# Kernel optimization log

Hardware: AMD Instinct MI355X
Metric: run time of the kernel (lower is better)

## Reference

```python
import jax, jax.numpy as jnp
import numpy as np

B, DEPTH, H, I = 8, 12, 512, 512
N = 2**DEPTH - 1  # 4095 nodes, complete binary tree (heap indexed)


def setup_inputs() -> dict:
    key = jax.random.key(0)
    ks = jax.random.split(key, 9)
    s_i = 1.0 / np.sqrt(I)
    s_h = 1.0 / np.sqrt(H)
    u = lambda k, shape, s: jax.random.uniform(k, shape, jnp.float32, -s, s)
    return {
        "inputs": jax.random.normal(ks[0], (B, N, I), jnp.float32),
        "depth": DEPTH,
        # torch Linear weights stored as [in, out] (already transposed)
        "W_gih": u(ks[1], (I, 3 * H), s_i),
        "b_gih": u(ks[2], (3 * H,), s_i),
        "W_glhh": u(ks[3], (H, 3 * H), s_h),
        "W_grhh": u(ks[4], (H, 3 * H), s_h),
        "W_cih": u(ks[5], (I, H), s_i),
        "b_cih": u(ks[6], (H,), s_i),
        "W_clhh": u(ks[7], (H, H), s_h),
        "W_crhh": u(ks[8], (H, H), s_h),
    }


def reference(inputs, depth, W_gih, b_gih, W_glhh, W_grhh, W_cih, b_cih, W_clhh, W_crhh):
    b, n, _ = inputs.shape
    h_dim = W_clhh.shape[0]
    # Input-dependent affines for every node, computed once (big GEMMs up front).
    gx = inputs @ W_gih + b_gih            # [B, N, 3H]
    cx = inputs @ W_cih + b_cih            # [B, N, H]

    def node_forward(gx_n, cx_n, lh, rh):
        # gates = sigmoid(gate_ih(x) + gate_lhh(lh) + gate_rhh(rh))
        gates = jax.nn.sigmoid(gx_n + lh @ W_glhh + rh @ W_grhh)
        rp, zp, z = jnp.split(gates, 3, axis=-1)
        cell = jnp.tanh(cx_n + (rp * lh) @ W_clhh + (rp * rh) @ W_crhh)
        return zp * (lh + rh) + z * cell

    h = jnp.zeros((b, n, h_dim), inputs.dtype)
    # root (node 0): both parent states are zeros
    z0 = jnp.zeros((b, h_dim), inputs.dtype)
    h = h.at[:, 0].set(node_forward(gx[:, 0], cx[:, 0], z0, z0))
    # top-down over levels; heap tree: parent(i)=(i-1)//2, odd index => left child
    for d in range(1, depth):
        start, end = 2 ** d - 1, 2 ** (d + 1) - 1
        idx = jnp.arange(start, end)
        parent = (idx - 1) // 2
        ph = h[:, parent]                          # [B, L, H] gather parent states
        is_left = (idx % 2 == 1)[None, :, None]
        lh = jnp.where(is_left, ph, jnp.zeros_like(ph))
        rh = jnp.where(is_left, jnp.zeros_like(ph), ph)
        h = h.at[:, start:end].set(node_forward(gx[:, start:end], cx[:, start:end], lh, rh))

    # original output ordering: nodes 1..N-1 then root; output_t = root state
    outputs = jnp.concatenate([h[:, 1:], h[:, :1]], axis=1)  # [B, N, H]
    return outputs, h[:, 0]
```

## Files before the change

### kernel.cpp

```cpp
#include <hip/hip_runtime.h>
#include <hip/hip_bf16.h>
#include <cstdint>
#include <cstddef>

#define BATCH   8
#define NNODES  4095
#define HD      512
#define ID      512
#define LDG     1536
#define MAXR    8192

typedef unsigned short ushort_t;
typedef __attribute__((ext_vector_type(8))) short  bf16x8;
typedef __attribute__((ext_vector_type(4))) float  f32x4;

__device__ __forceinline__ float bf2f(unsigned short u){
  union { uint32_t i; float f; } v; v.i = ((uint32_t)u) << 16; return v.f;
}
__device__ __forceinline__ unsigned short f2bf(float f){
  union { float f; uint32_t i; } v; v.f = f;
  uint32_t r = v.i + 0x7fffu + ((v.i >> 16) & 1u);
  return (unsigned short)(r >> 16);
}
__device__ __forceinline__ float sigm(float x){ return 1.0f/(1.0f + __expf(-x)); }
__device__ __forceinline__ float tanh_(float x){ return 1.0f - 2.0f/(__expf(2.0f*x)+1.0f); }

#define GLOAD16(g, l) __builtin_amdgcn_global_load_lds(                      \
    (const __attribute__((address_space(1))) void*)(g),                      \
    (__attribute__((address_space(3))) void*)(l), 16, 0, 0)

#define WAIT_VM(N)  asm volatile("s_waitcnt vmcnt(" #N ")" ::: "memory")
#define WAIT_LGKM0  asm volatile("s_waitcnt lgkmcnt(0)" ::: "memory")
#define SBAR        __builtin_amdgcn_s_barrier()
#define SCHEDB      __builtin_amdgcn_sched_barrier(0)

__device__ __forceinline__ int xcd_swz(int orig, int nwg){
  return (orig & 7) * (nwg >> 3) + (orig >> 3);
}



__global__ __launch_bounds__(256)
void prep_gather(const float* __restrict__ X, ushort_t* __restrict__ Abf,
                 const float* __restrict__ Wg_ih, const float* __restrict__ Wc_ih,
                 const float* __restrict__ Wg_l,  const float* __restrict__ Wg_r,
                 const float* __restrict__ Wc_l,  const float* __restrict__ Wc_r,
                 ushort_t* __restrict__ WgTih, ushort_t* __restrict__ WcTih,
                 ushort_t* __restrict__ WgThh, ushort_t* __restrict__ WcThh)
{
  __shared__ float t[64][65];
  const int bid = blockIdx.x;
  if (bid < 16380){
    const size_t i = (size_t)bid*256 + threadIdx.x;
    const int row = (int)(i >> 7);
    const int c4  = ((int)i & 127)*4;
    const int node = row >> 3, b = row & 7;
    float4 v = *(const float4*)&X[((size_t)b*NNODES + node)*ID + c4];
    ushort4 o = { f2bf(v.x), f2bf(v.y), f2bf(v.z), f2bf(v.w) };
    *(ushort4*)&Abf[(size_t)row*512 + c4] = o;
    return;
  }
  const int pid  = bid - 16380;
  const int px   = pid % 24;
  const int py   = (pid / 24) & 7;
  const int zsel = pid / 192;
  const float* W; ushort_t* D; int N;
  switch (zsel){
    case 0: W = Wg_ih; D = WgTih;                        N = 1536; break;
    case 1: W = Wc_ih; D = WcTih;                        N = 512;  break;
    case 2: W = Wg_l;  D = WgThh;                        N = 1536; break;
    case 3: W = Wg_r;  D = WgThh + (size_t)1536*512;     N = 1536; break;
    case 4: W = Wc_l;  D = WcThh;                        N = 512;  break;
    default:W = Wc_r;  D = WcThh + (size_t)512*512;      N = 512;  break;
  }
  const int n0 = px*64;
  if (n0 >= N) return;
  const int k0 = py*64;
  const int c = threadIdx.x & 63, rq = threadIdx.x >> 6;
  #pragma unroll
  for (int q = 0; q < 16; ++q){
    int r = q*4 + rq;
    t[r][c] = W[(size_t)(k0 + r)*N + n0 + c];
  }
  __syncthreads();
  #pragma unroll
  for (int q = 0; q < 16; ++q){
    int r = q*4 + rq;
    D[(size_t)(n0 + r)*512 + k0 + c] = f2bf(t[c][r]);
  }
}


#define READ_A(BUF, IH)                                                        \
  _Pragma("unroll") for (int i2_ = 0; i2_ < 4; ++i2_){                         \
    const int row_ = wr*128 + (IH)*64 + i2_*16 + fr;                           \
    _Pragma("unroll") for (int s_ = 0; s_ < 2; ++s_)                           \
      af[i2_][s_] = *(const bf16x8*)&Al[BUF][s_][row_][sl*8];                  \
  }

#define READ_B(BUF, JH, DST)                                                   \
  _Pragma("unroll") for (int j2_ = 0; j2_ < 2; ++j2_){                         \
    const int row_ = wc*64 + (JH)*32 + j2_*16 + fr;                            \
    _Pragma("unroll") for (int s_ = 0; s_ < 2; ++s_)                           \
      DST[j2_][s_] = *(const bf16x8*)&Bl[BUF][s_][row_][sl*8];                 \
  }

#define EXEC(IH, JH, BFR, STAGE_STMT, WAIT_STMT) do {                          \
  STAGE_STMT;                                                                  \
  SBAR;                                                                        \
  WAIT_LGKM0; SCHEDB;                                                          \
  __builtin_amdgcn_s_setprio(1);                                               \
  _Pragma("unroll") for (int i2_ = 0; i2_ < 4; ++i2_)                          \
    _Pragma("unroll") for (int j2_ = 0; j2_ < 2; ++j2_)                        \
      _Pragma("unroll") for (int s_ = 0; s_ < 2; ++s_)                         \
        acc[(IH)*4+i2_][(JH)*2+j2_] = __builtin_amdgcn_mfma_f32_16x16x32_bf16( \
            af[i2_][s_], BFR[j2_][s_], acc[(IH)*4+i2_][(JH)*2+j2_], 0,0,0);    \
  __builtin_amdgcn_s_setprio(0);                                               \
  WAIT_STMT;                                                                   \
  SCHEDB; SBAR;                                                                \
} while(0)

__global__ __launch_bounds__(512, 2)
void gemm_hoist(const ushort_t* __restrict__ A,
                const ushort_t* __restrict__ BTg, const float* __restrict__ bg,
                ushort_t* __restrict__ Gx,
                const ushort_t* __restrict__ BTc, const float* __restrict__ bc,
                ushort_t* __restrict__ Cx)
{
  __shared__ __align__(16) ushort_t SH[65536];
  ushort_t (*Al)[2][256][32] = (ushort_t (*)[2][256][32])SH;
  ushort_t (*Bl)[2][256][32] = (ushort_t (*)[2][256][32])(SH + 32768);
  const int wg = xcd_swz(blockIdx.x, gridDim.x);
  const ushort_t* BT; const float* bias; ushort_t* C; int N, m0, n0;
  if (wg < 768){ BT = BTg; bias = bg; C = Gx; N = 1536;
                 m0 = (wg/6)*256; n0 = (wg%6)*256; }
  else         { BT = BTc; bias = bc; C = Cx; N = 512;
                 const int t = wg - 768; m0 = (t>>1)*256; n0 = (t&1)*256; }
  const int tid = threadIdx.x, lane = tid & 63, wave = tid >> 6;
  const ushort_t* Abase = A + (size_t)m0*512;
  const ushort_t* Bbase = BT + (size_t)n0*512;
  const int wr = wave >> 2, wc = wave & 3;
  const int fr = lane & 15, fq = lane >> 4;
  const int lr = lane >> 2;
  const int cs = ((lane & 3) - (lr >> 1)) & 3;
  const size_t lo = (size_t)lr*512 + (size_t)cs*8;
  const int sl = (fq + (fr >> 1)) & 3;
  f32x4 acc[8][4] = {};
  bf16x8 af[4][2], bf0[2][2], bf1[2][2];

  auto stageA = [&](int buf, int h, int T){
    const int k0 = T*64;
    #pragma unroll
    for (int q = 0; q < 2; ++q){
      const int idx = wave*2 + q;
      const int s   = idx & 1;
      const int rb  = idx >> 1;
      const int r0  = (rb >> 2)*128 + h*64 + (rb & 3)*16;
      GLOAD16(Abase + (size_t)r0*512 + k0 + s*32 + lo, &Al[buf][s][r0][0]);
    }
  };
  auto stageB = [&](int buf, int h, int T){
    const int k0 = T*64;
    #pragma unroll
    for (int q = 0; q < 2; ++q){
      const int idx = wave*2 + q;
      const int s   = idx & 1;
      const int rb  = idx >> 1;
      const int r0  = (rb >> 1)*64 + h*32 + (rb & 1)*16;
      GLOAD16(Bbase + (size_t)r0*512 + k0 + s*32 + lo, &Bl[buf][s][r0][0]);
    }
  };

  stageA(0,0,0); stageB(0,0,0); stageA(0,1,0); stageB(0,1,0);
  stageA(1,0,1); stageB(1,0,1);
  WAIT_VM(4); SCHEDB; SBAR;

  for (int it = 0; it < 4; ++it){
    const int T1 = 2*it + 1, T2 = 2*it + 2, T3 = 2*it + 3;
    const bool more = (it < 3);
    READ_A(0,0); READ_B(0,0,bf0);
    EXEC(0,0,bf0, stageA(1,1,T1), (void)0);
    READ_B(0,1,bf1);
    EXEC(0,1,bf1, stageB(1,1,T1), (void)0);
    READ_A(0,1);
    EXEC(1,1,bf1, if(more) stageA(0,0,T2), (void)0);
    EXEC(1,0,bf0, if(more) stageB(0,0,T2),
                  if(more){ WAIT_VM(4); } else { WAIT_VM(0); });
    READ_A(1,0); READ_B(1,0,bf0);
    EXEC(0,0,bf0, if(more) stageA(0,1,T2), (void)0);
    READ_B(1,1,bf1);
    EXEC(0,1,bf1, if(more) stageB(0,1,T2), (void)0);
    READ_A(1,1);
    EXEC(1,1,bf1, if(more) stageA(1,0,T3), (void)0);
    EXEC(1,0,bf0, if(more) stageB(1,0,T3),
                  if(more){ WAIT_VM(4); } else { WAIT_VM(0); });
  }

  float* CT = (float*)SH;
  const int er = tid >> 3;
  const int ec = tid & 7;
  #pragma unroll
  for (int p = 0; p < 4; ++p){
    __syncthreads();
    #pragma unroll
    for (int i2 = 0; i2 < 2; ++i2){
      const int i = p*2 + i2;
      #pragma unroll
      for (int j = 0; j < 4; ++j){
        const int cc = wc*64 + j*16 + fr;
        const float bv = bias[n0 + cc];
        #pragma unroll
        for (int r = 0; r < 4; ++r){
          const int crow = wr*32 + i2*16 + fq*4 + r;
          CT[crow*256 + (cc ^ ((crow & 7) << 2))] = acc[i][j][r] + bv;
        }
      }
    }
    __syncthreads();
    const int grow = m0 + p*32 + (er >> 5)*128 + (er & 31);
    ushort_t* Crow = C + (size_t)grow*N + n0;
    const int rx = (er & 7) << 2;
    #pragma unroll
    for (int q = 0; q < 8; ++q){
      const int c0 = ec*4 + q*32;
      float4 v = *(const float4*)&CT[er*256 + (c0 ^ rx)];
      ushort4 o = { f2bf(v.x), f2bf(v.y), f2bf(v.z), f2bf(v.w) };
      *(ushort4*)&Crow[c0] = o;
    }
  }
}

__global__ __launch_bounds__(256)
void gates_rp(const ushort_t* __restrict__ Hprev, const ushort_t* __restrict__ WgThh,
              const ushort_t* __restrict__ Gx, ushort_t* __restrict__ Ubuf, int s)
{
  __shared__ __align__(16) ushort_t Al[3][128][32];
  __shared__ __align__(16) ushort_t Bl[3][128][32];
  const int wg = xcd_swz(blockIdx.x, gridDim.x);
  const int n0 = (wg & 3)*128;
  const int z  = (wg >> 2) & 1;
  const int m0 = (wg >> 3)*128;
  const int tid = threadIdx.x, lane = tid & 63, wave = tid >> 6;
  const ushort_t* Abase = Hprev + (size_t)m0*512;
  const ushort_t* Bbase = WgThh + ((size_t)z*1536 + n0)*512;
  const int wr = wave >> 1, wc = wave & 1;
  const int fr = lane & 15, fq = lane >> 4;
  const int lr = lane >> 2;
  const int cs = ((lane & 3) - (lr >> 1)) & 3;
  const size_t lo = (size_t)lr*512 + cs*8;
  const int sl = (fq + (fr >> 1)) & 3;
  f32x4 acc[4][4] = {};

  auto stage = [&](int buf, int kt){
    const int k0 = kt*32;
    #pragma unroll
    for (int q = 0; q < 2; ++q){
      int r = q*64 + wave*16;
      GLOAD16(Abase + (size_t)r*512 + k0 + lo, &Al[buf][r][0]);
      GLOAD16(Bbase + (size_t)r*512 + k0 + lo, &Bl[buf][r][0]);
    }
  };

  stage(0, 0); stage(1, 1); stage(2, 2);
  WAIT_VM(4); SCHEDB; SBAR;
  for (int it = 0; it < 8; ++it){
    const int cur = (2*it) % 3, nxt = (2*it + 1) % 3;
    bf16x8 af[4], bfr[4];
    #pragma unroll
    for (int i = 0; i < 4; i++){
      af[i]  = *(const bf16x8*)&Al[cur][wr*64 + i*16 + fr][sl*8];
      bfr[i] = *(const bf16x8*)&Bl[cur][wc*64 + i*16 + fr][sl*8];
    }
    WAIT_LGKM0; SCHEDB;
    __builtin_amdgcn_s_setprio(1);
    #pragma unroll
    for (int i = 0; i < 4; i++)
      #pragma unroll
      for (int j = 0; j < 4; j++)
        acc[i][j] = __builtin_amdgcn_mfma_f32_16x16x32_bf16(af[i], bfr[j], acc[i][j], 0,0,0);
    __builtin_amdgcn_s_setprio(0);
    #pragma unroll
    for (int i = 0; i < 4; i++){
      af[i]  = *(const bf16x8*)&Al[nxt][wr*64 + i*16 + fr][sl*8];
      bfr[i] = *(const bf16x8*)&Bl[nxt][wc*64 + i*16 + fr][sl*8];
    }
    WAIT_LGKM0; SCHEDB; SBAR;
    if (2*it + 3 < 16) stage(cur, 2*it + 3);
    if (2*it + 4 < 16) stage(nxt, 2*it + 4);
    __builtin_amdgcn_s_setprio(1);
    #pragma unroll
    for (int i = 0; i < 4; i++)
      #pragma unroll
      for (int j = 0; j < 4; j++)
        acc[i][j] = __builtin_amdgcn_mfma_f32_16x16x32_bf16(af[i], bfr[j], acc[i][j], 0,0,0);
    __builtin_amdgcn_s_setprio(0);
    if (2*it + 4 < 16){ WAIT_VM(4); } else { WAIT_VM(0); }
    SCHEDB; SBAR;
  }

  #pragma unroll
  for (int i = 0; i < 4; i++)
    #pragma unroll
    for (int j = 0; j < 4; j++){
      const int col = n0 + wc*64 + j*16 + fr;
      #pragma unroll
      for (int r = 0; r < 4; r++){
        const int m = m0 + wr*64 + i*16 + fq*4 + r;
        const int t = m >> 3, b = m & 7;
        const int node = s + 2*t + z;
        const float gx = bf2f(Gx[(size_t)(node*8 + b)*1536 + col]);
        const float ph = bf2f(Hprev[(size_t)m*512 + col]);
        Ubuf[((size_t)z*MAXR + m)*512 + col] = f2bf(sigm(acc[i][j][r] + gx) * ph);
      }
    }
}

__global__ __launch_bounds__(256)
void cell_comb(const ushort_t* __restrict__ Ubuf, const ushort_t* __restrict__ Hprev,
               const ushort_t* __restrict__ WcThh, const ushort_t* __restrict__ WgThh,
               const ushort_t* __restrict__ Gx, const ushort_t* __restrict__ Cx,
               float* __restrict__ out, ushort_t* __restrict__ Hcur,
               int s, int writeH)
{
  __shared__ __align__(16) ushort_t Ul[3][128][32];
  __shared__ __align__(16) ushort_t Hl[3][128][32];
  __shared__ __align__(16) ushort_t Bc[2][64][32];
  __shared__ __align__(16) ushort_t Bp[2][64][32];
  __shared__ __align__(16) ushort_t Bz[2][64][32];
  const int wg = xcd_swz(blockIdx.x, gridDim.x);
  const int n0 = (wg & 7)*64;
  const int z  = (wg >> 3) & 1;
  const int m0 = (wg >> 4)*128;
  const int tid = threadIdx.x, lane = tid & 63, wave = tid >> 6;
  const int wr = wave >> 1, wc = wave & 1;
  const int fr = lane & 15, fq = lane >> 4;
  const int lr = lane >> 2;
  const int cs = ((lane & 3) - (lr >> 1)) & 3;
  const int lc = cs*8;
  const int sl = (fq + (fr >> 1)) & 3;

  const ushort_t* Ab  = Ubuf  + ((size_t)z*MAXR + m0)*512;
  const ushort_t* Hb  = Hprev + (size_t)m0*512;
  const ushort_t* Bcb = WcThh + ((size_t)z*512  + n0)*512;
  const ushort_t* Bpb = WgThh + ((size_t)z*1536 + 512  + n0)*512;
  const ushort_t* Bzb = WgThh + ((size_t)z*1536 + 1024 + n0)*512;

  f32x4 acc_c[4][2] = {}, acc_p[4][2] = {}, acc_z[4][2] = {};

  auto stageA = [&](int buf, int kt){
    const int k0 = kt*32;
    #pragma unroll
    for (int q = 0; q < 2; ++q){
      const int r = q*64 + wave*16;
      GLOAD16(Ab + (size_t)(r + lr)*512 + k0 + lc, &Ul[buf][r][0]);
      GLOAD16(Hb + (size_t)(r + lr)*512 + k0 + lc, &Hl[buf][r][0]);
    }
  };
  auto stageB = [&](int buf, int kt){
    const int k0 = kt*32;
    const int r2 = wave*16;
    GLOAD16(Bcb + (size_t)(r2 + lr)*512 + k0 + lc, &Bc[buf][r2][0]);
    GLOAD16(Bpb + (size_t)(r2 + lr)*512 + k0 + lc, &Bp[buf][r2][0]);
    GLOAD16(Bzb + (size_t)(r2 + lr)*512 + k0 + lc, &Bz[buf][r2][0]);
  };

  auto read_frags = [&](int abuf, int bbuf, bf16x8 au[4], bf16x8 ah[4],
                        bf16x8 bc2[2], bf16x8 bp2[2], bf16x8 bz2[2]){
    #pragma unroll
    for (int i = 0; i < 4; i++){
      au[i] = *(const bf16x8*)&Ul[abuf][wr*64 + i*16 + fr][sl*8];
      ah[i] = *(const bf16x8*)&Hl[abuf][wr*64 + i*16 + fr][sl*8];
    }
    #pragma unroll
    for (int j = 0; j < 2; j++){
      bc2[j] = *(const bf16x8*)&Bc[bbuf][wc*32 + j*16 + fr][sl*8];
      bp2[j] = *(const bf16x8*)&Bp[bbuf][wc*32 + j*16 + fr][sl*8];
      bz2[j] = *(const bf16x8*)&Bz[bbuf][wc*32 + j*16 + fr][sl*8];
    }
  };

  stageB(0, 0); stageB(1, 1);
  stageA(0, 0); stageA(1, 1); stageA(2, 2);
  WAIT_VM(4); SCHEDB; SBAR;

  for (int it = 0; it < 8; ++it){
    const int a0 = (2*it) % 3, a1 = (2*it + 1) % 3;
    bf16x8 au[4], ah[4], bc2[2], bp2[2], bz2[2];
    read_frags(a0, 0, au, ah, bc2, bp2, bz2);
    WAIT_LGKM0; SCHEDB;
    __builtin_amdgcn_s_setprio(1);
    #pragma unroll
    for (int i = 0; i < 4; i++)
      #pragma unroll
      for (int j = 0; j < 2; j++){
        acc_c[i][j] = __builtin_amdgcn_mfma_f32_16x16x32_bf16(au[i], bc2[j], acc_c[i][j], 0,0,0);
        acc_p[i][j] = __builtin_amdgcn_mfma_f32_16x16x32_bf16(ah[i], bp2[j], acc_p[i][j], 0,0,0);
        acc_z[i][j] = __builtin_amdgcn_mfma_f32_16x16x32_bf16(ah[i], bz2[j], acc_z[i][j], 0,0,0);
      }
    __builtin_amdgcn_s_setprio(0);
    read_frags(a1, 1, au, ah, bc2, bp2, bz2);
    WAIT_LGKM0; SCHEDB; SBAR;
    if (2*it + 2 < 16) stageB(0, 2*it + 2);
    if (2*it + 3 < 16) stageB(1, 2*it + 3);
    if (2*it + 3 < 16) stageA(a0, 2*it + 3);
    if (2*it + 4 < 16) stageA(a1, 2*it + 4);
    __builtin_amdgcn_s_setprio(1);
    #pragma unroll
    for (int i = 0; i < 4; i++)
      #pragma unroll
      for (int j = 0; j < 2; j++){
        acc_c[i][j] = __builtin_amdgcn_mfma_f32_16x16x32_bf16(au[i], bc2[j], acc_c[i][j], 0,0,0);
        acc_p[i][j] = __builtin_amdgcn_mfma_f32_16x16x32_bf16(ah[i], bp2[j], acc_p[i][j], 0,0,0);
        acc_z[i][j] = __builtin_amdgcn_mfma_f32_16x16x32_bf16(ah[i], bz2[j], acc_z[i][j], 0,0,0);
      }
    __builtin_amdgcn_s_setprio(0);
    if (2*it + 4 < 16){ WAIT_VM(4); } else { WAIT_VM(0); }
    SCHEDB; SBAR;
  }

  #pragma unroll
  for (int i = 0; i < 4; i++)
    #pragma unroll
    for (int j = 0; j < 2; j++){
      const int col = n0 + wc*32 + j*16 + fr;
      #pragma unroll
      for (int r = 0; r < 4; r++){
        const int m = m0 + wr*64 + i*16 + fq*4 + r;
        const int t = m >> 3, b = m & 7;
        const int node = s + 2*t + z;
        const size_t crow = (size_t)node*8 + b;
        const float cell = tanh_(acc_c[i][j][r] + bf2f(Cx[crow*512 + col]));
        const float zp   = sigm(acc_p[i][j][r] + bf2f(Gx[crow*1536 + 512  + col]));
        const float zv   = sigm(acc_z[i][j][r] + bf2f(Gx[crow*1536 + 1024 + col]));
        const float ph = bf2f(Hprev[(size_t)m*512 + col]);
        const float h  = zp*ph + zv*cell;
        out[((size_t)b*NNODES + node - 1)*HD + col] = h;
        if (writeH) Hcur[(size_t)((2*t + z)*8 + b)*512 + col] = f2bf(h);
      }
    }
}

__global__ void root_k(const ushort_t* __restrict__ Gx, const ushort_t* __restrict__ Cx,
                       float* __restrict__ out, ushort_t* __restrict__ H0)
{
  const int b = blockIdx.x, c = threadIdx.x;
  float zv   = sigm(bf2f(Gx[(size_t)b*1536 + 1024 + c]));
  float cell = tanh_(bf2f(Cx[(size_t)b*512 + c]));
  float h = zv * cell;
  out[((size_t)b*NNODES + (NNODES-1))*HD + c] = h;
  out[(size_t)BATCH*NNODES*HD + (size_t)b*HD + c] = h;
  H0[(size_t)b*512 + c] = f2bf(h);
}

__global__ __launch_bounds__(1024)
void small_gates2(const ushort_t* __restrict__ Hprev, const ushort_t* __restrict__ Gx,
    const float* __restrict__ Wg_l, const float* __restrict__ Wg_r,
    float* __restrict__ G, float* __restrict__ Uf, int s)
{
  __shared__ float PHl[8][512];
  __shared__ float red[8][8][128];
  const int t = blockIdx.x, node = s + t;
  const int tid  = threadIdx.x;
  const int colq = tid & 127;
  const int ks   = tid >> 7;
  const int col  = blockIdx.y*128 + colq;
  const int prow0 = (t >> 1)*8;
  for (int idx = tid; idx < 8*512; idx += 1024){
    int b = idx >> 9, k = idx & 511;
    PHl[b][k] = bf2f(Hprev[(size_t)(prow0 + b)*512 + k]);
  }
  __syncthreads();
  const float* Whh = (node & 1) ? Wg_l : Wg_r;
  float acc[8] = {};
  const int k0 = ks << 6;
  #pragma unroll 8
  for (int k = 0; k < 64; k++){
    float w = Whh[(size_t)(k0 + k)*LDG + col];
    #pragma unroll
    for (int b = 0; b < 8; b++) acc[b] = fmaf(PHl[b][k0 + k], w, acc[b]);
  }
  #pragma unroll
  for (int b = 0; b < 8; b++) red[ks][b][colq] = acc[b];
  __syncthreads();
  if (ks == 0){
    #pragma unroll
    for (int b = 0; b < 8; b++){
      float a = bf2f(Gx[(size_t)(node*8 + b)*1536 + col]);
      #pragma unroll
      for (int q = 0; q < 8; q++) a += red[q][b][colq];
      float g = sigm(a);
      G[((size_t)(t*8 + b))*1536 + col] = g;
      if (col < 512) Uf[((size_t)(t*8 + b))*512 + col] = g * PHl[b][col];
    }
  }
}

__global__ __launch_bounds__(1024)
void small_cell2(float* __restrict__ out, const ushort_t* __restrict__ Cx,
    const float* __restrict__ Wc_l, const float* __restrict__ Wc_r,
    const float* __restrict__ G, const float* __restrict__ Uf,
    const ushort_t* __restrict__ Hprev, ushort_t* __restrict__ Hcur, int s)
{
  __shared__ float Ul[8][512];
  __shared__ float red[8][8][128];
  const int t = blockIdx.x, node = s + t;
  const int tid  = threadIdx.x;
  const int colq = tid & 127;
  const int ks   = tid >> 7;
  const int col  = blockIdx.y*128 + colq;
  for (int idx = tid; idx < 8*512; idx += 1024){
    int b = idx >> 9, k = idx & 511;
    Ul[b][k] = Uf[((size_t)(t*8 + b))*512 + k];
  }
  __syncthreads();
  const float* Whh = (node & 1) ? Wc_l : Wc_r;
  float acc[8] = {};
  const int k0 = ks << 6;
  #pragma unroll 8
  for (int k = 0; k < 64; k++){
    float w = Whh[(size_t)(k0 + k)*HD + col];
    #pragma unroll
    for (int b = 0; b < 8; b++) acc[b] = fmaf(Ul[b][k0 + k], w, acc[b]);
  }
  #pragma unroll
  for (int b = 0; b < 8; b++) red[ks][b][colq] = acc[b];
  __syncthreads();
  if (ks == 0){
    const int prow0 = (t >> 1)*8;
    #pragma unroll
    for (int b = 0; b < 8; b++){
      float a = bf2f(Cx[(size_t)(node*8 + b)*512 + col]);
      #pragma unroll
      for (int q = 0; q < 8; q++) a += red[q][b][colq];
      float zp = G[((size_t)(t*8 + b))*1536 + 512  + col];
      float zv = G[((size_t)(t*8 + b))*1536 + 1024 + col];
      float ph = bf2f(Hprev[(size_t)(prow0 + b)*512 + col]);
      float h  = zp*ph + zv*tanh_(a);
      out[((size_t)b*NNODES + (node - 1))*HD + col] = h;
      Hcur[(size_t)(t*8 + b)*512 + col] = f2bf(h);
    }
  }
}

__device__ __forceinline__ void unpack8(uint4 u, float v[8]){
  v[0]=bf2f((unsigned short)(u.x & 0xffffu)); v[1]=bf2f((unsigned short)(u.x >> 16));
  v[2]=bf2f((unsigned short)(u.y & 0xffffu)); v[3]=bf2f((unsigned short)(u.y >> 16));
  v[4]=bf2f((unsigned short)(u.z & 0xffffu)); v[5]=bf2f((unsigned short)(u.z >> 16));
  v[6]=bf2f((unsigned short)(u.w & 0xffffu)); v[7]=bf2f((unsigned short)(u.w >> 16));
}
__device__ __forceinline__ void gemm_acc(const unsigned short* Al0,
                                         const unsigned short* Al1,
                                         const float* __restrict__ W,
                                         int ldw, int c0, float acc[2][16])
{
  const float* wr = W + c0;
  #pragma unroll 2
  for (int k0 = 0; k0 < 512; k0 += 8){
    uint4 u0 = *(const uint4*)(Al0 + k0);
    uint4 u1 = *(const uint4*)(Al1 + k0);
    float a0[8], a1[8];
    unpack8(u0, a0); unpack8(u1, a1);
    #pragma unroll
    for (int kk = 0; kk < 8; kk++){
      float wv[16];
      *(float4*)(wv+ 0) = *(const float4*)(wr+ 0);
      *(float4*)(wv+ 4) = *(const float4*)(wr+ 4);
      *(float4*)(wv+ 8) = *(const float4*)(wr+ 8);
      *(float4*)(wv+12) = *(const float4*)(wr+12);
      wr += ldw;
      float x0 = a0[kk], x1 = a1[kk];
      #pragma unroll
      for (int j = 0; j < 16; j++){
        acc[0][j] = fmaf(x0, wv[j], acc[0][j]);
        acc[1][j] = fmaf(x1, wv[j], acc[1][j]);
      }
    }
  }
}

__global__ __launch_bounds__(256)
void tdtree_level(const float* __restrict__ X, float* __restrict__ out,
    const float* __restrict__ Wg_ih, const float* __restrict__ bg,
    const float* __restrict__ Wg_l,  const float* __restrict__ Wg_r,
    const float* __restrict__ Wc_ih, const float* __restrict__ bc,
    const float* __restrict__ Wc_l,  const float* __restrict__ Wc_r,
    int s, int nodes_p, int isRoot)
{
  __shared__ __align__(16) unsigned short Xl [16][512];
  __shared__ __align__(16) unsigned short PHl[16][512];
  __shared__ __align__(16) unsigned short Ul [16][512];

  const int tid = threadIdx.x;
  const int tx  = tid & 31;
  const int ty  = tid >> 5;
  const int parity = blockIdx.y;
  const float* Wg_hh = parity ? Wg_r : Wg_l;
  const float* Wc_hh = parity ? Wc_r : Wc_l;
  const int t0 = blockIdx.x * 2;

  for (int idx = tid; idx < 16*512; idx += 256){
    int m = idx >> 9, k = idx & 511;
    int t = t0 + (m >> 3), b = m & 7;
    float xv = 0.f, pv = 0.f;
    if (t < nodes_p){
      int node = isRoot ? 0 : (s + 2*t + parity);
      xv = X[((size_t)b*NNODES + node)*ID + k];
      if (!isRoot){
        int pnode = (node - 1) >> 1;
        int pslot = pnode ? (pnode - 1) : (NNODES - 1);
        pv = out[((size_t)b*NNODES + pslot)*HD + k];
      }
    }
    Xl[m][k]  = f2bf(xv);
    PHl[m][k] = f2bf(pv);
  }
  __syncthreads();

  const int r0 = ty*2, r1 = r0 + 1;
  const int c  = tx*16;
  const unsigned short* Ax0 = &Xl[r0][0];
  const unsigned short* Ax1 = &Xl[r1][0];
  const unsigned short* Ap0 = &PHl[r0][0];
  const unsigned short* Ap1 = &PHl[r1][0];
  float acc[2][16], cell[2][16];

  #pragma unroll
  for (int j=0;j<16;j++){ float bv = bg[c+j]; acc[0][j]=bv; acc[1][j]=bv; }
  gemm_acc(Ax0, Ax1, Wg_ih, LDG, c, acc);
  if (!isRoot) gemm_acc(Ap0, Ap1, Wg_hh, LDG, c, acc);
  #pragma unroll
  for (int j=0;j<16;j++){
    Ul[r0][c+j] = f2bf(sigm(acc[0][j]) * bf2f(PHl[r0][c+j]));
    Ul[r1][c+j] = f2bf(sigm(acc[1][j]) * bf2f(PHl[r1][c+j]));
  }
  __syncthreads();

  #pragma unroll
  for (int j=0;j<16;j++){ float bv = bc[c+j]; cell[0][j]=bv; cell[1][j]=bv; }
  gemm_acc(Ax0, Ax1, Wc_ih, HD, c, cell);
  if (!isRoot) gemm_acc(&Ul[r0][0], &Ul[r1][0], Wc_hh, HD, c, cell);
  #pragma unroll
  for (int j=0;j<16;j++){ cell[0][j] = tanh_(cell[0][j]); cell[1][j] = tanh_(cell[1][j]); }

  #pragma unroll
  for (int j=0;j<16;j++){ float bv = bg[1024+c+j]; acc[0][j]=bv; acc[1][j]=bv; }
  gemm_acc(Ax0, Ax1, Wg_ih, LDG, 1024+c, acc);
  if (!isRoot) gemm_acc(Ap0, Ap1, Wg_hh, LDG, 1024+c, acc);
  #pragma unroll
  for (int j=0;j<16;j++){ cell[0][j] *= sigm(acc[0][j]); cell[1][j] *= sigm(acc[1][j]); }

  #pragma unroll
  for (int j=0;j<16;j++){ float bv = bg[512+c+j]; acc[0][j]=bv; acc[1][j]=bv; }
  gemm_acc(Ax0, Ax1, Wg_ih, LDG, 512+c, acc);
  if (!isRoot) gemm_acc(Ap0, Ap1, Wg_hh, LDG, 512+c, acc);

  #pragma unroll
  for (int i=0;i<2;i++){
    int m = r0 + i;
    int t = t0 + (m >> 3), b = m & 7;
    if (t >= nodes_p) continue;
    int node = isRoot ? 0 : (s + 2*t + parity);
    int slot = node ? (node - 1) : (NNODES - 1);
    float* op = out + ((size_t)b*NNODES + slot)*HD + c;
    float hv[16];
    if (isRoot){
      #pragma unroll
      for (int j=0;j<16;j++) hv[j] = cell[i][j];
    } else {
      int pnode = (node - 1) >> 1;
      int pslot = pnode ? (pnode - 1) : (NNODES - 1);
      const float* pp = out + ((size_t)b*NNODES + pslot)*HD + c;
      #pragma unroll
      for (int j=0;j<16;j++) hv[j] = sigm(acc[i][j]) * pp[j] + cell[i][j];
    }
    #pragma unroll
    for (int q=0;q<4;q++) *(float4*)(op + q*4) = *(const float4*)(hv + q*4);
    if (isRoot){
      float* o2 = out + (size_t)BATCH*NNODES*HD + (size_t)b*HD + c;
      #pragma unroll
      for (int q=0;q<4;q++) *(float4*)(o2 + q*4) = *(const float4*)(hv + q*4);
    }
  }
}

extern "C" void kernel_launch(void* const* d_in, const int* in_sizes, int n_in,
                              void* d_out, int out_size, void* d_ws, size_t ws_size,
                              hipStream_t stream)
{
  const float* X     = (const float*)d_in[0];
  const float* Wg_ih = (const float*)d_in[2];
  const float* bg    = (const float*)d_in[3];
  const float* Wg_l  = (const float*)d_in[4];
  const float* Wg_r  = (const float*)d_in[5];
  const float* Wc_ih = (const float*)d_in[6];
  const float* bc    = (const float*)d_in[7];
  const float* Wc_l  = (const float*)d_in[8];
  const float* Wc_r  = (const float*)d_in[9];
  float* out = (float*)d_out;
  char* ws = (char*)d_ws;

  size_t o = 0;
  ushort_t* WgTih = (ushort_t*)(ws + o); o += (size_t)1536*512*2;
  ushort_t* WcTih = (ushort_t*)(ws + o); o += (size_t)512*512*2;
  ushort_t* WgThh = (ushort_t*)(ws + o); o += (size_t)3072*512*2;
  ushort_t* WcThh = (ushort_t*)(ws + o); o += (size_t)1024*512*2;
  ushort_t* Gxp   = (ushort_t*)(ws + o); o += (size_t)32768*1536*2;
  ushort_t* Cxp   = (ushort_t*)(ws + o); o += (size_t)32768*512*2;
  ushort_t* Hb0   = (ushort_t*)(ws + o); o += (size_t)MAXR*512*2;
  ushort_t* Hb1   = (ushort_t*)(ws + o); o += (size_t)MAXR*512*2;
  char*     BIG   = ws + o;              o += (size_t)32768*512*2;
  float*    Gs    = (float*)(ws + o);    o += (size_t)512*1536*4;
  float*    Us    = (float*)(ws + o);    o += (size_t)512*512*4;
  const size_t NEED = o;

  if (ws_size >= NEED){
    ushort_t* Abf  = (ushort_t*)BIG;
    ushort_t* Ubuf = (ushort_t*)BIG;

    prep_gather<<<dim3(16380 + 1152), 256, 0, stream>>>(
        X, Abf, Wg_ih, Wc_ih, Wg_l, Wg_r, Wc_l, Wc_r,
        WgTih, WcTih, WgThh, WcThh);
    gemm_hoist<<<dim3(1024), 512, 0, stream>>>(Abf, WgTih, bg, Gxp, WcTih, bc, Cxp);

    root_k<<<dim3(8), 512, 0, stream>>>(Gxp, Cxp, out, Hb0);

    for (int d = 1; d < 12; ++d){
      const int count = 1 << d, s = count - 1;
      ushort_t* Hprev = ((d-1) & 1) ? Hb1 : Hb0;
      ushort_t* Hcur  = (d & 1) ? Hb1 : Hb0;
      if (d < 7){
        small_gates2<<<dim3(count,12), 1024, 0, stream>>>(Hprev, Gxp, Wg_l, Wg_r, Gs, Us, s);
        small_cell2 <<<dim3(count,4),  1024, 0, stream>>>(out, Cxp, Wc_l, Wc_r, Gs, Us, Hprev, Hcur, s);
      } else {
        const int mt = 1 << (d - 5);
        gates_rp <<<dim3(mt*8),  256, 0, stream>>>(Hprev, WgThh, Gxp, Ubuf, s);
        cell_comb<<<dim3(mt*16), 256, 0, stream>>>(Ubuf, Hprev, WcThh, WgThh,
                                                   Gxp, Cxp, out, Hcur, s, d < 11);
      }
    }
    return;
  }

  for (int d = 0; d < 12; ++d){
    const int count  = 1 << d;
    const int snode  = count - 1;
    const int isRoot = (d == 0);
    const int nodes_p = isRoot ? 1 : (count >> 1);
    const int blocks  = (nodes_p + 1) >> 1;
    dim3 grid(blocks, isRoot ? 1 : 2);
    tdtree_level<<<grid, 256, 0, stream>>>(X, out, Wg_ih, bg, Wg_l, Wg_r,
                                           Wc_ih, bc, Wc_l, Wc_r,
                                           snode, nodes_p, isRoot);
  }
}
```

Baseline: 543.0 us.

## Replace ping-pong staged GEMM pipeline with simple BK=32 double buffer

The input-projection GEMM drops its interleaved half-tile schedule, which staged A and B in 64-wide K chunks split into halves and overlapped loads with MFMA groups. It now uses a plain double-buffered loop over 32-wide K tiles: each step loads all fragments, runs 32 MFMAs, then stages the tile two steps ahead. Shared memory per block is halved, which may allow two blocks per CU as the launch bounds request and reduces code complexity. In exchange, each step has more barriers per unit of work and less overlap between global loads and math.

```diff
diff --git a/kernel.cpp b/kernel.cpp
--- a/kernel.cpp
+++ b/kernel.cpp
@@ -90,36 +90,6 @@
   }
 }
 
-
-#define READ_A(BUF, IH)                                                        \
-  _Pragma("unroll") for (int i2_ = 0; i2_ < 4; ++i2_){                         \
-    const int row_ = wr*128 + (IH)*64 + i2_*16 + fr;                           \
-    _Pragma("unroll") for (int s_ = 0; s_ < 2; ++s_)                           \
-      af[i2_][s_] = *(const bf16x8*)&Al[BUF][s_][row_][sl*8];                  \
-  }
-
-#define READ_B(BUF, JH, DST)                                                   \
-  _Pragma("unroll") for (int j2_ = 0; j2_ < 2; ++j2_){                         \
-    const int row_ = wc*64 + (JH)*32 + j2_*16 + fr;                            \
-    _Pragma("unroll") for (int s_ = 0; s_ < 2; ++s_)                           \
-      DST[j2_][s_] = *(const bf16x8*)&Bl[BUF][s_][row_][sl*8];                 \
-  }
-
-#define EXEC(IH, JH, BFR, STAGE_STMT, WAIT_STMT) do {                          \
-  STAGE_STMT;                                                                  \
-  SBAR;                                                                        \
-  WAIT_LGKM0; SCHEDB;                                                          \
-  __builtin_amdgcn_s_setprio(1);                                               \
-  _Pragma("unroll") for (int i2_ = 0; i2_ < 4; ++i2_)                          \
-    _Pragma("unroll") for (int j2_ = 0; j2_ < 2; ++j2_)                        \
-      _Pragma("unroll") for (int s_ = 0; s_ < 2; ++s_)                         \
-        acc[(IH)*4+i2_][(JH)*2+j2_] = __builtin_amdgcn_mfma_f32_16x16x32_bf16( \
-            af[i2_][s_], BFR[j2_][s_], acc[(IH)*4+i2_][(JH)*2+j2_], 0,0,0);    \
-  __builtin_amdgcn_s_setprio(0);                                               \
-  WAIT_STMT;                                                                   \
-  SCHEDB; SBAR;                                                                \
-} while(0)
-
 __global__ __launch_bounds__(512, 2)
 void gemm_hoist(const ushort_t* __restrict__ A,
                 const ushort_t* __restrict__ BTg, const float* __restrict__ bg,
@@ -127,9 +97,9 @@
                 const ushort_t* __restrict__ BTc, const float* __restrict__ bc,
                 ushort_t* __restrict__ Cx)
 {
-  __shared__ __align__(16) ushort_t SH[65536];
-  ushort_t (*Al)[2][256][32] = (ushort_t (*)[2][256][32])SH;
-  ushort_t (*Bl)[2][256][32] = (ushort_t (*)[2][256][32])(SH + 32768);
+  __shared__ __align__(16) ushort_t SH[32768];
+  ushort_t (*Al)[256][32] = (ushort_t (*)[256][32])SH;
+  ushort_t (*Bl)[256][32] = (ushort_t (*)[256][32])(SH + 16384);
   const int wg = xcd_swz(blockIdx.x, gridDim.x);
   const ushort_t* BT; const float* bias; ushort_t* C; int N, m0, n0;
   if (wg < 768){ BT = BTg; bias = bg; C = Gx; N = 1536;
@@ -146,54 +116,41 @@
   const size_t lo = (size_t)lr*512 + (size_t)cs*8;
   const int sl = (fq + (fr >> 1)) & 3;
   f32x4 acc[8][4] = {};
-  bf16x8 af[4][2], bf0[2][2], bf1[2][2];
-
-  auto stageA = [&](int buf, int h, int T){
-    const int k0 = T*64;
+
+  auto stage = [&](int buf, int kt){
+    const int k0 = kt*32;
     #pragma unroll
     for (int q = 0; q < 2; ++q){
-      const int idx = wave*2 + q;
-      const int s   = idx & 1;
-      const int rb  = idx >> 1;
-      const int r0  = (rb >> 2)*128 + h*64 + (rb & 3)*16;
-      GLOAD16(Abase + (size_t)r0*512 + k0 + s*32 + lo, &Al[buf][s][r0][0]);
+      const int r0 = (wave*2 + q)*16;
+      GLOAD16(Abase + (size_t)r0*512 + k0 + lo, &Al[buf][r0][0]);
+      GLOAD16(Bbase + (size_t)r0*512 + k0 + lo, &Bl[buf][r0][0]);
     }
   };
-  auto stageB = [&](int buf, int h, int T){
-    const int k0 = T*64;
-    #pragma unroll
-    for (int q = 0; q < 2; ++q){
-      const int idx = wave*2 + q;
-      const int s   = idx & 1;
-      const int rb  = idx >> 1;
-      const int r0  = (rb >> 1)*64 + h*32 + (rb & 1)*16;
-      GLOAD16(Bbase + (size_t)r0*512 + k0 + s*32 + lo, &Bl[buf][s][r0][0]);
-    }
-  };
-
-  stageA(0,0,0); stageB(0,0,0); stageA(0,1,0); stageB(0,1,0);
-  stageA(1,0,1); stageB(1,0,1);
+
+  stage(0, 0); stage(1, 1);
   WAIT_VM(4); SCHEDB; SBAR;
-
-  for (int it = 0; it < 4; ++it){
-    const int T1 = 2*it + 1, T2 = 2*it + 2, T3 = 2*it + 3;
-    const bool more = (it < 3);
-    READ_A(0,0); READ_B(0,0,bf0);
-    EXEC(0,0,bf0, stageA(1,1,T1), (void)0);
-    READ_B(0,1,bf1);
-    EXEC(0,1,bf1, stageB(1,1,T1), (void)0);
-    READ_A(0,1);
-    EXEC(1,1,bf1, if(more) stageA(0,0,T2), (void)0);
-    EXEC(1,0,bf0, if(more) stageB(0,0,T2),
-                  if(more){ WAIT_VM(4); } else { WAIT_VM(0); });
-    READ_A(1,0); READ_B(1,0,bf0);
-    EXEC(0,0,bf0, if(more) stageA(0,1,T2), (void)0);
-    READ_B(1,1,bf1);
-    EXEC(0,1,bf1, if(more) stageB(0,1,T2), (void)0);
-    READ_A(1,1);
-    EXEC(1,1,bf1, if(more) stageA(1,0,T3), (void)0);
-    EXEC(1,0,bf0, if(more) stageB(1,0,T3),
-                  if(more){ WAIT_VM(4); } else { WAIT_VM(0); });
+  int cur = 0;
+  for (int kt = 0; kt < 16; ++kt){
+    bf16x8 af[8], bfr[4];
+    #pragma unroll
+    for (int i = 0; i < 8; i++)
+      af[i] = *(const bf16x8*)&Al[cur][wr*128 + i*16 + fr][sl*8];
+    #pragma unroll
+    for (int j = 0; j < 4; j++)
+      bfr[j] = *(const bf16x8*)&Bl[cur][wc*64 + j*16 + fr][sl*8];
+    WAIT_LGKM0; SCHEDB;
+    __builtin_amdgcn_s_setprio(1);
+    #pragma unroll
+    for (int i = 0; i < 8; i++)
+      #pragma unroll
+      for (int j = 0; j < 4; j++)
+        acc[i][j] = __builtin_amdgcn_mfma_f32_16x16x32_bf16(af[i], bfr[j], acc[i][j], 0,0,0);
+    __builtin_amdgcn_s_setprio(0);
+    SCHEDB; SBAR;
+    if (kt < 14) stage(cur, kt + 2);
+    if (kt < 14) { WAIT_VM(4); } else { WAIT_VM(0); }
+    SCHEDB; SBAR;
+    cur ^= 1;
   }
 
   float* CT = (float*)SH;
```

Result: faster. 531.0 us, median of 2 (-2.2%).
